# Optimization experiments

Hardware: AMD Instinct MI355X
Metric: run time of the kernel (lower is better)

Reference implementation:

```python
import jax, jax.numpy as jnp
import numpy as np

N, E, D, A, M, H, NRES = 65536, 16384, 1024, 512, 2048, 3, 3


def setup_inputs() -> dict:
    key = jax.random.key(0)
    ks = jax.random.split(key, 24)
    s = 0.02
    inp = {
        'h': jax.random.normal(ks[0], (N, D), dtype=jnp.float32),
        'rep': jax.random.normal(ks[1], (N, D), dtype=jnp.float32),
        'src': jax.random.randint(ks[2], (E,), 0, N, dtype=jnp.int32),
        'dst': jax.random.randint(ks[3], (E,), 0, N, dtype=jnp.int32),
        # per-head attention projections (stacked over H heads)
        'Wq': s * jax.random.normal(ks[4], (H, D, A), dtype=jnp.float32),
        'bq': s * jax.random.normal(ks[5], (H, A), dtype=jnp.float32),
        'Wk': s * jax.random.normal(ks[6], (H, D, A), dtype=jnp.float32),
        'bk': s * jax.random.normal(ks[7], (H, A), dtype=jnp.float32),
        'Wv': s * jax.random.normal(ks[8], (H, D, A), dtype=jnp.float32),
        'bv': s * jax.random.normal(ks[9], (H, A), dtype=jnp.float32),
        # MultiMLPLayer: first Linear(A->M), then NRES ResNet blocks of width M
        'W0': s * jax.random.normal(ks[10], (H, A, M), dtype=jnp.float32),
        'b0': s * jax.random.normal(ks[11], (H, M), dtype=jnp.float32),
        'Wr': s * jax.random.normal(ks[12], (H, NRES, M, M), dtype=jnp.float32),
        'br': s * jax.random.normal(ks[13], (H, NRES, M), dtype=jnp.float32),
        'g_ln': jnp.ones((H, NRES, M), dtype=jnp.float32),
        'b_ln': jnp.zeros((H, NRES, M), dtype=jnp.float32),
        # mlp_scale: Linear(M->A) per head
        'Wms': s * jax.random.normal(ks[14], (H, M, A), dtype=jnp.float32),
        'bms': s * jax.random.normal(ks[15], (H, A), dtype=jnp.float32),
        # update_attn_scale: Linear(H*A -> D, bias=False)
        'Wuas': s * jax.random.normal(ks[16], (H * A, D), dtype=jnp.float32),
    }
    return inp


def _layernorm(x, g, b, eps=1e-5):
    mu = jnp.mean(x, axis=-1, keepdims=True)
    var = jnp.mean((x - mu) ** 2, axis=-1, keepdims=True)
    return (x - mu) / jnp.sqrt(var + eps) * g + b


def reference(h, rep, src, dst, Wq, bq, Wk, bk, Wv, bv, W0, b0, Wr, br,
              g_ln, b_ln, Wms, bms, Wuas):
    # model normalizes all node embeddings first (F.normalize)
    hn = h / jnp.maximum(jnp.linalg.norm(h, axis=-1, keepdims=True), 1e-12)
    Q = hn[src]            # [E, D] mailbox messages (copy_u of 'h')
    K = rep[dst]           # [E, D] destination node reps (K == V)

    # per-head projections: [H, E, A]
    Qp = jnp.einsum('ed,hda->hea', Q, Wq) + bq[:, None, :]
    Kp = jnp.einsum('ed,hda->hea', K, Wk) + bk[:, None, :]
    Vp = jnp.einsum('ed,hda->hea', K, Wv) + bv[:, None, :]

    attn_dim = Wq.shape[-1]
    scores = (Qp * Kp) / (attn_dim ** 0.5)       # 2D path: elementwise QK, scaled by sqrt(attn_size)
    attn = jax.nn.softmax(scores, axis=-1)       # softmax over feature dim
    attn_out = attn * Vp                         # [H, E, A] (dropout p=0.0 in TreeHopNode)

    # MultiMLPLayer: Linear(A->M) then NRES ResNet blocks
    m = jnp.einsum('hea,ham->hem', attn_out, W0) + b0[:, None, :]
    for j in range(Wr.shape[1]):
        xn = _layernorm(m, g_ln[:, j][:, None, :], b_ln[:, j][:, None, :])
        m = m + jax.nn.relu(jnp.einsum('hem,hmn->hen', xn, Wr[:, j]) + br[:, j][:, None, :])

    head_out = jnp.einsum('hem,hma->hea', m, Wms) + bms[:, None, :] + attn_out  # [H, E, A]
    cat = jnp.transpose(head_out, (1, 0, 2)).reshape(Q.shape[0], -1)            # [E, H*A]

    # reduce_func: h = Q - K + update_attn_scale(multi_head_out)
    return Q - K + cat @ Wuas                                                   # [E, D]
```

## Files before the change

### kernel.cpp

```cpp
#include <hip/hip_runtime.h>
#include <hip/hip_bf16.h>
#include <cstdint>
#include <cstddef>

typedef __bf16 bf16;
typedef __bf16 bf16x2 __attribute__((ext_vector_type(2)));
typedef __bf16 bf16x4 __attribute__((ext_vector_type(4)));
typedef __bf16 bf16x8 __attribute__((ext_vector_type(8)));
typedef float f32x4 __attribute__((ext_vector_type(4)));

static_assert(sizeof(bf16x8) == 16, "bf16x8 must be 16B");

#define NE 16384
#define ND 1024
#define NA 512
#define NM 2048
#define NH 3
#define NRES 3
#define ESH 14

__device__ __forceinline__ void async_ld16(const bf16* g, bf16* l) {
  __builtin_amdgcn_global_load_lds(
      (__attribute__((address_space(1))) void*)(void*)g,
      (__attribute__((address_space(3))) void*)(void*)l, 16, 0, 0);
}

template <int N>
__device__ __forceinline__ void vm_wait() {
  asm volatile("s_waitcnt vmcnt(%0)" ::"n"(N) : "memory");
}
__device__ __forceinline__ void lgkm0() {
  asm volatile("s_waitcnt lgkmcnt(0)" ::: "memory");
}
__device__ __forceinline__ void bar() {
  asm volatile("s_barrier" ::: "memory");
}
#define PIN() __builtin_amdgcn_sched_barrier(0)


#define LDA_H(KS, BUF, MQ)                                                    \
  {                                                                           \
    const int ab_ = ((BUF)*2 + (MQ)) * 8192 + aOff;                           \
    const int co_ = (c0 ^ ((KS) << 2)) * 8;                                   \
    _Pragma("unroll") for (int i = 0; i < 4; ++i)                             \
        fa[KS][i] = *(const bf16x8*)&lA[ab_ + i * 1024 + co_];                \
  }

#define LDB_H(DST, KS, BUF, NQ)                                               \
  {                                                                           \
    const int bb_ = ((BUF)*2 + (NQ)) * 8192 + bOff;                           \
    const int co_ = (c0 ^ ((KS) << 2)) * 8;                                   \
    _Pragma("unroll") for (int j = 0; j < 2; ++j)                             \
        DST[KS][j] = *(const bf16x8*)&lB[bb_ + j * 1024 + co_];               \
  }

#define MFMA_H(KS, MQ, NQ, FB)                                                \
  __builtin_amdgcn_s_setprio(1);                                              \
  _Pragma("unroll") for (int i = 0; i < 4; ++i)                               \
  _Pragma("unroll") for (int j = 0; j < 2; ++j)                               \
      acc[(MQ)*4 + i][(NQ)*2 + j] = __builtin_amdgcn_mfma_f32_16x16x32_bf16(  \
          fa[KS][i], FB[KS][j], acc[(MQ)*4 + i][(NQ)*2 + j], 0, 0, 0);        \
  __builtin_amdgcn_s_setprio(0);

template <int MODE>
__global__ __launch_bounds__(512, 2) void gemm_kernel(
    const bf16* __restrict__ A, const bf16* __restrict__ B,
    const float* __restrict__ bias, void* __restrict__ Cv,
    const bf16* __restrict__ addb, int K, int ldc, int coloff, int addld,
    int nbx, int hsh, long long bstr, int bistr) {
  __shared__ bf16 lA[32768];
  __shared__ bf16 lB[32768];

  const int nwg = gridDim.x;
  int bid = blockIdx.x;
  if ((nwg & 7) == 0) bid = (bid & 7) * (nwg >> 3) + (bid >> 3);
  const int n0 = (bid % nbx) * 256;
  const int m0 = (bid / nbx) * 256;

  const int hidx = hsh ? (m0 >> hsh) : 0;
  if (hsh) {
    B += (size_t)hidx * (size_t)bstr;
    bias += (size_t)hidx * (size_t)bistr;
  }

  const int tid = threadIdx.x;
  const int wv = tid >> 6, ln = tid & 63;
  const int wm = wv >> 2, wn = wv & 3;

  const int rowq = wv * 8 + (ln >> 3);
  const int colo = ((ln & 7) ^ (ln >> 3)) * 8;
  const bf16* gA = A + (size_t)(m0 + rowq) * K + colo;
  const bf16* gB = B + (size_t)(n0 + rowq) * K + colo;

  auto stageA = [&](int bf, int u, int t) {
#pragma unroll
    for (int r = 0; r < 2; ++r)
      async_ld16(gA + (size_t)(r * 128 + u * 64) * K + t * 64,
                 &lA[((bf * 2 + u) * 128 + r * 64 + wv * 8) * 64]);
  };
  auto stageB = [&](int bf, int u, int t) {
#pragma unroll
    for (int r = 0; r < 2; ++r)
      async_ld16(gB + (size_t)(r * 128 + u * 64) * K + t * 64,
                 &lB[((bf * 2 + u) * 128 + r * 64 + wv * 8) * 64]);
  };

  const int l15 = ln & 15;
  const int aOff = (wm * 64 + l15) * 64;
  const int bOff = (wn * 32 + l15) * 64;
  const int c0 = (ln >> 4) ^ (ln & 7);

  f32x4 acc[8][4] = {};
  bf16x8 fa[2][4], fb0[2][2], fb1[2][2];

  const int nt = K >> 6;

  stageA(0, 0, 0); stageA(0, 1, 0); stageB(0, 0, 0); stageB(0, 1, 0);
  stageA(1, 0, 1); stageA(1, 1, 1); stageB(1, 0, 1); stageB(1, 1, 1);
  vm_wait<8>();
  bar();
  LDA_H(0, 0, 0); LDA_H(1, 0, 0); LDB_H(fb0, 0, 0, 0); LDB_H(fb0, 1, 0, 0);
  lgkm0();
  bar();

  for (int t = 0; t < nt; ++t) {
    const int buf = t & 1, nb = buf ^ 1;
    const bool s1 = t + 1 < nt, s2 = t + 2 < nt;
    if (s2) { stageB(buf, 0, t + 2); stageA(buf, 0, t + 2); }
    PIN();
    LDB_H(fb1, 0, buf, 1); LDB_H(fb1, 1, buf, 1);
    PIN();
    MFMA_H(0, 0, 0, fb0);
    MFMA_H(1, 0, 0, fb0);
    MFMA_H(0, 0, 1, fb1);
    PIN();
    LDA_H(0, buf, 1);
    PIN();
    MFMA_H(1, 0, 1, fb1);
    PIN();
    LDA_H(1, buf, 1);
    lgkm0();
    bar();
    if (s2) { stageB(buf, 1, t + 2); stageA(buf, 1, t + 2); }
    PIN();
    MFMA_H(0, 1, 1, fb1);
    MFMA_H(1, 1, 1, fb1);
    if (s2) { vm_wait<8>(); } else if (s1) { vm_wait<0>(); }
    bar();
    MFMA_H(0, 1, 0, fb0);
    PIN();
    if (s1) { LDB_H(fb0, 0, nb, 0); LDA_H(0, nb, 0); }
    PIN();
    MFMA_H(1, 1, 0, fb0);
    PIN();
    if (s1) { LDB_H(fb0, 1, nb, 0); LDA_H(1, nb, 0); }
    lgkm0();
    bar();
  }

  const int r4 = (ln >> 4) * 4;
  const int nbase = n0 + (wn >> 1) * 128 + (wn & 1) * 32 + l15;
#pragma unroll
  for (int mi = 0; mi < 8; ++mi) {
#pragma unroll
    for (int ni = 0; ni < 4; ++ni) {
#pragma unroll
      for (int r = 0; r < 4; ++r) {
        const int m = m0 + wm * 128 + mi * 16 + r4 + r;
        const int n = nbase + (ni >> 1) * 64 + (ni & 1) * 16;
        float v = acc[mi][ni][r];
        if constexpr (MODE != 3) v += bias[n];
        if constexpr (MODE == 0) {
          size_t idx = (size_t)m * ldc + n;
          if (coloff && n >= coloff) idx += (size_t)addld;
          ((bf16*)Cv)[idx] = (bf16)v;
        } else if constexpr (MODE == 1) {
          float prev = (float)addb[(size_t)m * addld + n];
          ((bf16*)Cv)[(size_t)m * ldc + n] = (bf16)(prev + fmaxf(v, 0.f));
        } else if constexpr (MODE == 2) {
          v += (float)addb[(size_t)m * addld + n];
          const int mloc = hsh ? (m & ((1 << hsh) - 1)) : m;
          ((bf16*)Cv)[(size_t)mloc * ldc + hidx * coloff + n] = (bf16)v;
        } else {
          float* C = (float*)Cv;
          const size_t idx = (size_t)m * ldc + n;
          C[idx] = C[idx] + v;
        }
      }
    }
  }
}

template <int MODE>
static void launch_gemm(hipStream_t s, const bf16* A, const bf16* B,
                        const float* bias, void* C, const bf16* addb, int M,
                        int N, int K, int ldc, int coloff, int addld,
                        int hsh = 0, long long bstr = 0, int bistr = 0) {
  const int nbx = N / 256;
  gemm_kernel<MODE><<<dim3(nbx * (M / 256)), 512, 0, s>>>(
      A, B, bias, C, addb, K, ldc, coloff, addld, nbx, hsh, bstr, bistr);
}

__global__ void transpose_cvt(const float* __restrict__ src,
                              bf16* __restrict__ dst, int K, int N) {
  __shared__ float t[32][33];
  const size_t zo = (size_t)blockIdx.z * K * N;
  src += zo;
  dst += zo;
  const int n = blockIdx.x * 32 + threadIdx.x;
  const int kb = blockIdx.y * 32;
#pragma unroll
  for (int i = 0; i < 4; ++i) {
    const int k = kb + threadIdx.y + i * 8;
    t[threadIdx.y + i * 8][threadIdx.x] = src[(size_t)k * N + n];
  }
  __syncthreads();
#pragma unroll
  for (int i = 0; i < 4; ++i) {
    const int nn = blockIdx.x * 32 + threadIdx.y + i * 8;
    dst[(size_t)nn * K + kb + threadIdx.x] =
        (bf16)t[threadIdx.x][threadIdx.y + i * 8];
  }
}

__global__ void concat2_kernel(const float* __restrict__ a,
                               const float* __restrict__ b,
                               float* __restrict__ dst, int na) {
  const int i = blockIdx.x * 256 + threadIdx.x;
  dst[i] = (i < na) ? a[i] : b[i - na];
}

__global__ __launch_bounds__(256) void gather_kernel(
    const float* __restrict__ h, const float* __restrict__ rep,
    const int* __restrict__ src, const int* __restrict__ dst,
    bf16* __restrict__ Qb, bf16* __restrict__ Kb, float* __restrict__ qk) {
  __shared__ float sm[4];
  const int e = blockIdx.x, tid = threadIdx.x;
  const int sr = src[e], dr = dst[e];
  const float4 hv = ((const float4*)(h + (size_t)sr * ND))[tid];
  float ss = hv.x * hv.x + hv.y * hv.y + hv.z * hv.z + hv.w * hv.w;
#pragma unroll
  for (int o = 32; o > 0; o >>= 1) ss += __shfl_down(ss, o, 64);
  if ((tid & 63) == 0) sm[tid >> 6] = ss;
  __syncthreads();
  const float tot = sm[0] + sm[1] + sm[2] + sm[3];
  const float inv = 1.f / fmaxf(sqrtf(tot), 1e-12f);
  const float4 rv = ((const float4*)(rep + (size_t)dr * ND))[tid];
  const float q0 = hv.x * inv, q1 = hv.y * inv, q2 = hv.z * inv,
              q3 = hv.w * inv;
  const size_t base = (size_t)e * ND + tid * 4;
  bf16x4 qv;
  qv[0] = (bf16)q0; qv[1] = (bf16)q1; qv[2] = (bf16)q2; qv[3] = (bf16)q3;
  *(bf16x4*)(Qb + base) = qv;
  bf16x4 kv;
  kv[0] = (bf16)rv.x; kv[1] = (bf16)rv.y; kv[2] = (bf16)rv.z;
  kv[3] = (bf16)rv.w;
  *(bf16x4*)(Kb + base) = kv;
  *(float4*)(qk + base) =
      make_float4(q0 - rv.x, q1 - rv.y, q2 - rv.z, q3 - rv.w);
}

__global__ __launch_bounds__(256) void softmax_kernel(
    const bf16* __restrict__ Qp, const bf16* __restrict__ Kp,
    const bf16* __restrict__ Vp, bf16* __restrict__ attn) {
  __shared__ float sm[4];
  const int tid = threadIdx.x;
  const int e = blockIdx.x, hh = blockIdx.y;
  const size_t base = (size_t)e * (NH * NA) + (size_t)hh * NA + 2 * tid;
  const bf16x2 q = *(const bf16x2*)(Qp + base);
  const bf16x2 k = *(const bf16x2*)(Kp + base);
  const bf16x2 v = *(const bf16x2*)(Vp + base);
  const float sc = 0.044194173824159216f;
  const float s0 = (float)q[0] * (float)k[0] * sc;
  const float s1 = (float)q[1] * (float)k[1] * sc;
  float mx = fmaxf(s0, s1);
#pragma unroll
  for (int o = 32; o > 0; o >>= 1) mx = fmaxf(mx, __shfl_down(mx, o, 64));
  if ((tid & 63) == 0) sm[tid >> 6] = mx;
  __syncthreads();
  mx = fmaxf(fmaxf(sm[0], sm[1]), fmaxf(sm[2], sm[3]));
  __syncthreads();
  const float p0 = expf(s0 - mx), p1 = expf(s1 - mx);
  float ssum = p0 + p1;
#pragma unroll
  for (int o = 32; o > 0; o >>= 1) ssum += __shfl_down(ssum, o, 64);
  if ((tid & 63) == 0) sm[tid >> 6] = ssum;
  __syncthreads();
  const float inv = 1.f / (sm[0] + sm[1] + sm[2] + sm[3]);
  bf16x2 r;
  r[0] = (bf16)(p0 * inv * (float)v[0]);
  r[1] = (bf16)(p1 * inv * (float)v[1]);
  const size_t obase = (size_t)hh * NE * NA + (size_t)e * NA + 2 * tid;
  *(bf16x2*)(attn + obase) = r;
}

__global__ __launch_bounds__(256) void ln_kernel(const bf16* __restrict__ x,
                                                 bf16* __restrict__ y,
                                                 const float* __restrict__ g,
                                                 const float* __restrict__ b) {
  __shared__ float sm[8];
  const int tid = threadIdx.x;
  const size_t base = (size_t)blockIdx.x * NM + tid * 8;
  const bf16x8 xv = *(const bf16x8*)(x + base);
  float xf[8], s = 0.f, ss = 0.f;
#pragma unroll
  for (int i = 0; i < 8; ++i) {
    xf[i] = (float)xv[i];
    s += xf[i];
    ss += xf[i] * xf[i];
  }
#pragma unroll
  for (int o = 32; o > 0; o >>= 1) {
    s += __shfl_down(s, o, 64);
    ss += __shfl_down(ss, o, 64);
  }
  if ((tid & 63) == 0) {
    sm[tid >> 6] = s;
    sm[4 + (tid >> 6)] = ss;
  }
  __syncthreads();
  s = sm[0] + sm[1] + sm[2] + sm[3];
  ss = sm[4] + sm[5] + sm[6] + sm[7];
  const float mu = s * (1.f / NM);
  const float var = ss * (1.f / NM) - mu * mu;
  const float rstd = rsqrtf(fmaxf(var, 0.f) + 1e-5f);
  const int c0 = tid * 8;
  bf16x8 yv;
#pragma unroll
  for (int i = 0; i < 8; ++i)
    yv[i] = (bf16)((xf[i] - mu) * rstd * g[c0 + i] + b[c0 + i]);
  *(bf16x8*)(y + base) = yv;
}

extern "C" void kernel_launch(void* const* d_in, const int* in_sizes, int n_in,
                              void* d_out, int out_size, void* d_ws,
                              size_t ws_size, hipStream_t stream) {
  const float* h    = (const float*)d_in[0];
  const float* rep  = (const float*)d_in[1];
  const int* src    = (const int*)d_in[2];
  const int* dst    = (const int*)d_in[3];
  const float* Wq   = (const float*)d_in[4];
  const float* bq   = (const float*)d_in[5];
  const float* Wk   = (const float*)d_in[6];
  const float* bk   = (const float*)d_in[7];
  const float* Wv   = (const float*)d_in[8];
  const float* bv   = (const float*)d_in[9];
  const float* W0   = (const float*)d_in[10];
  const float* b0   = (const float*)d_in[11];
  const float* Wr   = (const float*)d_in[12];
  const float* br   = (const float*)d_in[13];
  const float* g_ln = (const float*)d_in[14];
  const float* b_ln = (const float*)d_in[15];
  const float* Wms  = (const float*)d_in[16];
  const float* bms  = (const float*)d_in[17];
  const float* Wuas = (const float*)d_in[18];
  float* out = (float*)d_out;

  bf16* ws = (bf16*)d_ws;
  size_t off = 0;
  auto alloc = [&](size_t n) {
    bf16* p = ws + off;
    off += n;
    return p;
  };
  bf16* WqT   = alloc((size_t)NH * NA * ND);
  bf16* WkT   = alloc((size_t)NH * NA * ND);
  bf16* WvT   = alloc((size_t)NH * NA * ND);
  bf16* W0T   = alloc((size_t)NH * NM * NA);
  bf16* WrT   = alloc((size_t)NH * NRES * NM * NM);
  bf16* WmsT  = alloc((size_t)NH * NA * NM);
  bf16* WuasT = alloc((size_t)ND * NH * NA);
  bf16* Qb    = alloc((size_t)NE * ND);
  bf16* Kb    = alloc((size_t)NE * ND);
  bf16* Qp    = alloc((size_t)NE * NH * NA);
  bf16* Kp    = alloc((size_t)NE * NH * NA);
  bf16* Vp    = alloc((size_t)NE * NH * NA);
  bf16* attn  = alloc((size_t)NH * NE * NA);
  bf16* mbuf3 = alloc((size_t)NH * NE * NM);
  bf16* xnb   = alloc((size_t)NE * NM);
  float* cbias = (float*)alloc(2 * (size_t)NH * NA * 2);
  bf16* cat   = Qp;
  if (ws_size < off * sizeof(bf16)) return;

  const dim3 tb(32, 8);
  transpose_cvt<<<dim3(NA / 32, ND / 32, NH), tb, 0, stream>>>(Wq, WqT, ND, NA);
  transpose_cvt<<<dim3(NA / 32, ND / 32, NH), tb, 0, stream>>>(Wk, WkT, ND, NA);
  transpose_cvt<<<dim3(NA / 32, ND / 32, NH), tb, 0, stream>>>(Wv, WvT, ND, NA);
  transpose_cvt<<<dim3(NM / 32, NA / 32, NH), tb, 0, stream>>>(W0, W0T, NA, NM);
  transpose_cvt<<<dim3(NM / 32, NM / 32, NH * NRES), tb, 0, stream>>>(Wr, WrT,
                                                                      NM, NM);
  transpose_cvt<<<dim3(NA / 32, NM / 32, NH), tb, 0, stream>>>(Wms, WmsT, NM,
                                                               NA);
  transpose_cvt<<<dim3(ND / 32, (NH * NA) / 32, 1), tb, 0, stream>>>(
      Wuas, WuasT, NH * NA, ND);
  concat2_kernel<<<(2 * NH * NA) / 256, 256, 0, stream>>>(bk, bv, cbias,
                                                          NH * NA);

  gather_kernel<<<NE, 256, 0, stream>>>(h, rep, src, dst, Qb, Kb, out);

  launch_gemm<0>(stream, Qb, WqT, bq, Qp, nullptr, NE, NH * NA, ND, NH * NA,
                 0, 0);
  launch_gemm<0>(stream, Kb, WkT, cbias, Kp, nullptr, NE, 2 * NH * NA, ND,
                 NH * NA, NH * NA, (NE - 1) * NH * NA);
  softmax_kernel<<<dim3(NE, NH), 256, 0, stream>>>(Qp, Kp, Vp, attn);

  for (int hh = 0; hh < NH; ++hh) {
    const bf16* attn_h = attn + (size_t)hh * NE * NA;
    bf16* mbuf_h = mbuf3 + (size_t)hh * NE * NM;
    launch_gemm<0>(stream, attn_h, W0T + (size_t)hh * NM * NA, b0 + hh * NM,
                   mbuf_h, nullptr, NE, NM, NA, NM, 0, 0);
    for (int j = 0; j < NRES; ++j) {
      const int hj = hh * NRES + j;
      ln_kernel<<<NE, 256, 0, stream>>>(mbuf_h, xnb, g_ln + (size_t)hj * NM,
                                        b_ln + (size_t)hj * NM);
      launch_gemm<1>(stream, xnb, WrT + (size_t)hj * NM * NM, br + hj * NM,
                     mbuf_h, mbuf_h, NE, NM, NM, NM, 0, NM);
    }
  }
  launch_gemm<2>(stream, mbuf3, WmsT, bms, cat, attn, NH * NE, NA, NM,
                 NH * NA, NA, NA, ESH, (long long)NA * NM, NA);

  launch_gemm<3>(stream, cat, WuasT, nullptr, out, nullptr, NE, ND, NH * NA,
                 ND, 0, 0);
}
```

Measured before the change: 2.606 ms.

## Fold LayerNorm into ResNet GEMMs via weight scaling and epilogue row statistics

Removes the standalone LayerNorm kernel. Gamma is folded into the transposed Wr weights, and mean and beta are folded into precomputed column sums (sgW and bWbr). The GEMM epilogue applies rstd*(acc - mu*sgW) + bWbr, using per-row sum and sum-of-squares that the previous GEMM epilogue accumulates with atomics. This drops a full read and write of the activation buffer per residual block, at the cost of atomic traffic in the epilogue. It also adds numerical risk, since the raw un-normalized bf16 activations now feed the MFMA.

```diff
diff --git a/kernel.cpp b/kernel.cpp
--- a/kernel.cpp
+++ b/kernel.cpp
@@ -67,7 +67,9 @@
     const bf16* __restrict__ A, const bf16* __restrict__ B,
     const float* __restrict__ bias, void* __restrict__ Cv,
     const bf16* __restrict__ addb, int K, int ldc, int coloff, int addld,
-    int nbx, int hsh, long long bstr, int bistr) {
+    int nbx, int hsh, long long bstr, int bistr,
+    const float* __restrict__ lnbb, const float* __restrict__ stats_in,
+    float* __restrict__ stats_out) {
   __shared__ bf16 lA[32768];
   __shared__ bf16 lB[32768];
 
@@ -163,21 +165,34 @@
 #pragma unroll
   for (int mi = 0; mi < 8; ++mi) {
 #pragma unroll
-    for (int ni = 0; ni < 4; ++ni) {
-#pragma unroll
-      for (int r = 0; r < 4; ++r) {
-        const int m = m0 + wm * 128 + mi * 16 + r4 + r;
+    for (int r = 0; r < 4; ++r) {
+      const int m = m0 + wm * 128 + mi * 16 + r4 + r;
+      float mu = 0.f, rstd = 0.f;
+      if constexpr (MODE == 1) {
+        const float2 st = *(const float2*)&stats_in[2 * m];
+        mu = st.x * (1.f / NM);
+        const float var = st.y * (1.f / NM) - mu * mu;
+        rstd = rsqrtf(fmaxf(var, 0.f) + 1e-5f);
+      }
+      float s = 0.f, sq = 0.f;
+#pragma unroll
+      for (int ni = 0; ni < 4; ++ni) {
         const int n = nbase + (ni >> 1) * 64 + (ni & 1) * 16;
         float v = acc[mi][ni][r];
-        if constexpr (MODE != 3) v += bias[n];
         if constexpr (MODE == 0) {
+          v += bias[n];
           size_t idx = (size_t)m * ldc + n;
           if (coloff && n >= coloff) idx += (size_t)addld;
           ((bf16*)Cv)[idx] = (bf16)v;
+          s += v; sq += v * v;
         } else if constexpr (MODE == 1) {
-          float prev = (float)addb[(size_t)m * addld + n];
-          ((bf16*)Cv)[(size_t)m * ldc + n] = (bf16)(prev + fmaxf(v, 0.f));
+          v = rstd * (v - mu * bias[n]) + lnbb[n];
+          const float prev = (float)addb[(size_t)m * addld + n];
+          const float y = prev + fmaxf(v, 0.f);
+          ((bf16*)Cv)[(size_t)m * ldc + n] = (bf16)y;
+          s += y; sq += y * y;
         } else if constexpr (MODE == 2) {
+          v += bias[n];
           v += (float)addb[(size_t)m * addld + n];
           const int mloc = hsh ? (m & ((1 << hsh) - 1)) : m;
           ((bf16*)Cv)[(size_t)mloc * ldc + hidx * coloff + n] = (bf16)v;
@@ -187,6 +202,19 @@
           C[idx] = C[idx] + v;
         }
       }
+      if constexpr (MODE <= 1) {
+        if (stats_out) {
+#pragma unroll
+          for (int o = 1; o < 16; o <<= 1) {
+            s += __shfl_xor(s, o, 64);
+            sq += __shfl_xor(sq, o, 64);
+          }
+          if (l15 == 0) {
+            atomicAdd(&stats_out[2 * m], s);
+            atomicAdd(&stats_out[2 * m + 1], sq);
+          }
+        }
+      }
     }
   }
 }
@@ -195,16 +223,22 @@
 static void launch_gemm(hipStream_t s, const bf16* A, const bf16* B,
                         const float* bias, void* C, const bf16* addb, int M,
                         int N, int K, int ldc, int coloff, int addld,
-                        int hsh = 0, long long bstr = 0, int bistr = 0) {
+                        int hsh = 0, long long bstr = 0, int bistr = 0,
+                        const float* lnbb = nullptr,
+                        const float* stats_in = nullptr,
+                        float* stats_out = nullptr) {
   const int nbx = N / 256;
   gemm_kernel<MODE><<<dim3(nbx * (M / 256)), 512, 0, s>>>(
-      A, B, bias, C, addb, K, ldc, coloff, addld, nbx, hsh, bstr, bistr);
+      A, B, bias, C, addb, K, ldc, coloff, addld, nbx, hsh, bstr, bistr,
+      lnbb, stats_in, stats_out);
 }
 
 __global__ void transpose_cvt(const float* __restrict__ src,
-                              bf16* __restrict__ dst, int K, int N) {
+                              bf16* __restrict__ dst, int K, int N,
+                              const float* __restrict__ scale) {
   __shared__ float t[32][33];
-  const size_t zo = (size_t)blockIdx.z * K * N;
+  const int z = blockIdx.z;
+  const size_t zo = (size_t)z * K * N;
   src += zo;
   dst += zo;
   const int n = blockIdx.x * 32 + threadIdx.x;
@@ -215,12 +249,37 @@
     t[threadIdx.y + i * 8][threadIdx.x] = src[(size_t)k * N + n];
   }
   __syncthreads();
+  const float sc = scale ? scale[(size_t)z * K + kb + threadIdx.x] : 1.f;
 #pragma unroll
   for (int i = 0; i < 4; ++i) {
     const int nn = blockIdx.x * 32 + threadIdx.y + i * 8;
     dst[(size_t)nn * K + kb + threadIdx.x] =
-        (bf16)t[threadIdx.x][threadIdx.y + i * 8];
-  }
+        (bf16)(t[threadIdx.x][threadIdx.y + i * 8] * sc);
+  }
+}
+
+__global__ void lnfold_kernel(const float* __restrict__ Wr,
+                              const float* __restrict__ g,
+                              const float* __restrict__ b,
+                              const float* __restrict__ br,
+                              float* __restrict__ sgW,
+                              float* __restrict__ bWbr) {
+  const int hj = blockIdx.y;
+  const int n = blockIdx.x * 256 + threadIdx.x;
+  const float* W = Wr + (size_t)hj * NM * NM;
+  float sg = 0.f, sb = 0.f;
+  for (int k = 0; k < NM; ++k) {
+    const float w = W[(size_t)k * NM + n];
+    sg += g[hj * NM + k] * w;
+    sb += b[hj * NM + k] * w;
+  }
+  sgW[hj * NM + n] = sg;
+  bWbr[hj * NM + n] = sb + br[hj * NM + n];
+}
+
+__global__ void zerof_kernel(float* __restrict__ p, int n) {
+  const int i = blockIdx.x * 256 + threadIdx.x;
+  if (i < n) p[i] = 0.f;
 }
 
 __global__ void concat2_kernel(const float* __restrict__ a,
@@ -292,44 +351,6 @@
   r[1] = (bf16)(p1 * inv * (float)v[1]);
   const size_t obase = (size_t)hh * NE * NA + (size_t)e * NA + 2 * tid;
   *(bf16x2*)(attn + obase) = r;
-}
-
-__global__ __launch_bounds__(256) void ln_kernel(const bf16* __restrict__ x,
-                                                 bf16* __restrict__ y,
-                                                 const float* __restrict__ g,
-                                                 const float* __restrict__ b) {
-  __shared__ float sm[8];
-  const int tid = threadIdx.x;
-  const size_t base = (size_t)blockIdx.x * NM + tid * 8;
-  const bf16x8 xv = *(const bf16x8*)(x + base);
-  float xf[8], s = 0.f, ss = 0.f;
-#pragma unroll
-  for (int i = 0; i < 8; ++i) {
-    xf[i] = (float)xv[i];
-    s += xf[i];
-    ss += xf[i] * xf[i];
-  }
-#pragma unroll
-  for (int o = 32; o > 0; o >>= 1) {
-    s += __shfl_down(s, o, 64);
-    ss += __shfl_down(ss, o, 64);
-  }
-  if ((tid & 63) == 0) {
-    sm[tid >> 6] = s;
-    sm[4 + (tid >> 6)] = ss;
-  }
-  __syncthreads();
-  s = sm[0] + sm[1] + sm[2] + sm[3];
-  ss = sm[4] + sm[5] + sm[6] + sm[7];
-  const float mu = s * (1.f / NM);
-  const float var = ss * (1.f / NM) - mu * mu;
-  const float rstd = rsqrtf(fmaxf(var, 0.f) + 1e-5f);
-  const int c0 = tid * 8;
-  bf16x8 yv;
-#pragma unroll
-  for (int i = 0; i < 8; ++i)
-    yv[i] = (bf16)((xf[i] - mu) * rstd * g[c0 + i] + b[c0 + i]);
-  *(bf16x8*)(y + base) = yv;
 }
 
 extern "C" void kernel_launch(void* const* d_in, const int* in_sizes, int n_in,
@@ -377,24 +398,33 @@
   bf16* Vp    = alloc((size_t)NE * NH * NA);
   bf16* attn  = alloc((size_t)NH * NE * NA);
   bf16* mbuf3 = alloc((size_t)NH * NE * NM);
-  bf16* xnb   = alloc((size_t)NE * NM);
-  float* cbias = (float*)alloc(2 * (size_t)NH * NA * 2);
+  float* cbias  = (float*)alloc(2 * (size_t)NH * NA * 2);
+  float* sgW    = (float*)alloc((size_t)NH * NRES * NM * 2);
+  float* bWbr   = (float*)alloc((size_t)NH * NRES * NM * 2);
+  float* stats9 = (float*)alloc((size_t)9 * NE * 2 * 2);
   bf16* cat   = Qp;
   if (ws_size < off * sizeof(bf16)) return;
 
   const dim3 tb(32, 8);
-  transpose_cvt<<<dim3(NA / 32, ND / 32, NH), tb, 0, stream>>>(Wq, WqT, ND, NA);
-  transpose_cvt<<<dim3(NA / 32, ND / 32, NH), tb, 0, stream>>>(Wk, WkT, ND, NA);
-  transpose_cvt<<<dim3(NA / 32, ND / 32, NH), tb, 0, stream>>>(Wv, WvT, ND, NA);
-  transpose_cvt<<<dim3(NM / 32, NA / 32, NH), tb, 0, stream>>>(W0, W0T, NA, NM);
-  transpose_cvt<<<dim3(NM / 32, NM / 32, NH * NRES), tb, 0, stream>>>(Wr, WrT,
-                                                                      NM, NM);
+  transpose_cvt<<<dim3(NA / 32, ND / 32, NH), tb, 0, stream>>>(Wq, WqT, ND, NA,
+                                                               nullptr);
+  transpose_cvt<<<dim3(NA / 32, ND / 32, NH), tb, 0, stream>>>(Wk, WkT, ND, NA,
+                                                               nullptr);
+  transpose_cvt<<<dim3(NA / 32, ND / 32, NH), tb, 0, stream>>>(Wv, WvT, ND, NA,
+                                                               nullptr);
+  transpose_cvt<<<dim3(NM / 32, NA / 32, NH), tb, 0, stream>>>(W0, W0T, NA, NM,
+                                                               nullptr);
+  transpose_cvt<<<dim3(NM / 32, NM / 32, NH * NRES), tb, 0, stream>>>(
+      Wr, WrT, NM, NM, g_ln);
   transpose_cvt<<<dim3(NA / 32, NM / 32, NH), tb, 0, stream>>>(Wms, WmsT, NM,
-                                                               NA);
+                                                               NA, nullptr);
   transpose_cvt<<<dim3(ND / 32, (NH * NA) / 32, 1), tb, 0, stream>>>(
-      Wuas, WuasT, NH * NA, ND);
+      Wuas, WuasT, NH * NA, ND, nullptr);
   concat2_kernel<<<(2 * NH * NA) / 256, 256, 0, stream>>>(bk, bv, cbias,
                                                           NH * NA);
+  lnfold_kernel<<<dim3(NM / 256, NH * NRES), 256, 0, stream>>>(
+      Wr, g_ln, b_ln, br, sgW, bWbr);
+  zerof_kernel<<<(9 * NE * 2) / 256, 256, 0, stream>>>(stats9, 9 * NE * 2);
 
   gather_kernel<<<NE, 256, 0, stream>>>(h, rep, src, dst, Qb, Kb, out);
 
@@ -407,14 +437,18 @@
   for (int hh = 0; hh < NH; ++hh) {
     const bf16* attn_h = attn + (size_t)hh * NE * NA;
     bf16* mbuf_h = mbuf3 + (size_t)hh * NE * NM;
+    float* S[3] = {stats9 + (size_t)(hh * 3 + 0) * NE * 2,
+                   stats9 + (size_t)(hh * 3 + 1) * NE * 2,
+                   stats9 + (size_t)(hh * 3 + 2) * NE * 2};
     launch_gemm<0>(stream, attn_h, W0T + (size_t)hh * NM * NA, b0 + hh * NM,
-                   mbuf_h, nullptr, NE, NM, NA, NM, 0, 0);
+                   mbuf_h, nullptr, NE, NM, NA, NM, 0, 0, 0, 0, 0, nullptr,
+                   nullptr, S[0]);
     for (int j = 0; j < NRES; ++j) {
       const int hj = hh * NRES + j;
-      ln_kernel<<<NE, 256, 0, stream>>>(mbuf_h, xnb, g_ln + (size_t)hj * NM,
-                                        b_ln + (size_t)hj * NM);
-      launch_gemm<1>(stream, xnb, WrT + (size_t)hj * NM * NM, br + hj * NM,
-                     mbuf_h, mbuf_h, NE, NM, NM, NM, 0, NM);
+      launch_gemm<1>(stream, mbuf_h, WrT + (size_t)hj * NM * NM,
+                     sgW + (size_t)hj * NM, mbuf_h, mbuf_h, NE, NM, NM, NM, 0,
+                     NM, 0, 0, 0, bWbr + (size_t)hj * NM, S[j],
+                     j + 1 < NRES ? S[j + 1] : nullptr);
     }
   }
   launch_gemm<2>(stream, mbuf3, WmsT, bms, cat, attn, NH * NE, NA, NM,
```

New measurement: 2.960 ms. 13.6% more time.

## Replace 256x256 pipelined GEMM with simpler 128x128 single-buffered tile kernel

Applied to the files above, without the earlier changes.

Replaces the hand-scheduled 256x256 tile, 8-wave, double-buffered GEMM with a 128x128 tile, 4-wave kernel. It uses a single LDS buffer, with a full vmcnt wait and barrier each K step. The intent appears to be more workgroups per CU and simpler scheduling in exchange for less data reuse per tile. The risk is that global loads and MFMA no longer overlap well, and the fine-grained interleaving that hid LDS latency is gone.

```diff
diff --git a/kernel.cpp b/kernel.cpp
--- a/kernel.cpp
+++ b/kernel.cpp
@@ -35,47 +35,22 @@
 __device__ __forceinline__ void bar() {
   asm volatile("s_barrier" ::: "memory");
 }
-#define PIN() __builtin_amdgcn_sched_barrier(0)
-
-
-#define LDA_H(KS, BUF, MQ)                                                    \
-  {                                                                           \
-    const int ab_ = ((BUF)*2 + (MQ)) * 8192 + aOff;                           \
-    const int co_ = (c0 ^ ((KS) << 2)) * 8;                                   \
-    _Pragma("unroll") for (int i = 0; i < 4; ++i)                             \
-        fa[KS][i] = *(const bf16x8*)&lA[ab_ + i * 1024 + co_];                \
-  }
-
-#define LDB_H(DST, KS, BUF, NQ)                                               \
-  {                                                                           \
-    const int bb_ = ((BUF)*2 + (NQ)) * 8192 + bOff;                           \
-    const int co_ = (c0 ^ ((KS) << 2)) * 8;                                   \
-    _Pragma("unroll") for (int j = 0; j < 2; ++j)                             \
-        DST[KS][j] = *(const bf16x8*)&lB[bb_ + j * 1024 + co_];               \
-  }
-
-#define MFMA_H(KS, MQ, NQ, FB)                                                \
-  __builtin_amdgcn_s_setprio(1);                                              \
-  _Pragma("unroll") for (int i = 0; i < 4; ++i)                               \
-  _Pragma("unroll") for (int j = 0; j < 2; ++j)                               \
-      acc[(MQ)*4 + i][(NQ)*2 + j] = __builtin_amdgcn_mfma_f32_16x16x32_bf16(  \
-          fa[KS][i], FB[KS][j], acc[(MQ)*4 + i][(NQ)*2 + j], 0, 0, 0);        \
-  __builtin_amdgcn_s_setprio(0);
+
 
 template <int MODE>
-__global__ __launch_bounds__(512, 2) void gemm_kernel(
+__global__ __launch_bounds__(256, 3) void gemm_kernel(
     const bf16* __restrict__ A, const bf16* __restrict__ B,
     const float* __restrict__ bias, void* __restrict__ Cv,
     const bf16* __restrict__ addb, int K, int ldc, int coloff, int addld,
     int nbx, int hsh, long long bstr, int bistr) {
-  __shared__ bf16 lA[32768];
-  __shared__ bf16 lB[32768];
+  __shared__ bf16 lA[8192];
+  __shared__ bf16 lB[8192];
 
   const int nwg = gridDim.x;
   int bid = blockIdx.x;
   if ((nwg & 7) == 0) bid = (bid & 7) * (nwg >> 3) + (bid >> 3);
-  const int n0 = (bid % nbx) * 256;
-  const int m0 = (bid / nbx) * 256;
+  const int n0 = (bid % nbx) * 128;
+  const int m0 = (bid / nbx) * 128;
 
   const int hidx = hsh ? (m0 >> hsh) : 0;
   if (hsh) {
@@ -85,89 +60,73 @@
 
   const int tid = threadIdx.x;
   const int wv = tid >> 6, ln = tid & 63;
-  const int wm = wv >> 2, wn = wv & 3;
+  const int wm = wv >> 1, wn = wv & 1;
 
   const int rowq = wv * 8 + (ln >> 3);
   const int colo = ((ln & 7) ^ (ln >> 3)) * 8;
   const bf16* gA = A + (size_t)(m0 + rowq) * K + colo;
   const bf16* gB = B + (size_t)(n0 + rowq) * K + colo;
 
-  auto stageA = [&](int bf, int u, int t) {
-#pragma unroll
-    for (int r = 0; r < 2; ++r)
-      async_ld16(gA + (size_t)(r * 128 + u * 64) * K + t * 64,
-                 &lA[((bf * 2 + u) * 128 + r * 64 + wv * 8) * 64]);
-  };
-  auto stageB = [&](int bf, int u, int t) {
-#pragma unroll
-    for (int r = 0; r < 2; ++r)
-      async_ld16(gB + (size_t)(r * 128 + u * 64) * K + t * 64,
-                 &lB[((bf * 2 + u) * 128 + r * 64 + wv * 8) * 64]);
+  auto stage = [&](int t) {
+#pragma unroll
+    for (int r = 0; r < 4; ++r) {
+      async_ld16(gA + (size_t)(r * 32) * K + t * 64,
+                 &lA[(r * 32 + wv * 8) * 64]);
+      async_ld16(gB + (size_t)(r * 32) * K + t * 64,
+                 &lB[(r * 32 + wv * 8) * 64]);
+    }
   };
 
   const int l15 = ln & 15;
   const int aOff = (wm * 64 + l15) * 64;
-  const int bOff = (wn * 32 + l15) * 64;
+  const int bOff = (wn * 64 + l15) * 64;
   const int c0 = (ln >> 4) ^ (ln & 7);
 
-  f32x4 acc[8][4] = {};
-  bf16x8 fa[2][4], fb0[2][2], fb1[2][2];
+  f32x4 acc[4][4] = {};
+  bf16x8 fa[2][4], fb[2][4];
 
   const int nt = K >> 6;
 
-  stageA(0, 0, 0); stageA(0, 1, 0); stageB(0, 0, 0); stageB(0, 1, 0);
-  stageA(1, 0, 1); stageA(1, 1, 1); stageB(1, 0, 1); stageB(1, 1, 1);
-  vm_wait<8>();
-  bar();
-  LDA_H(0, 0, 0); LDA_H(1, 0, 0); LDB_H(fb0, 0, 0, 0); LDB_H(fb0, 1, 0, 0);
-  lgkm0();
-  bar();
+  stage(0);
 
   for (int t = 0; t < nt; ++t) {
-    const int buf = t & 1, nb = buf ^ 1;
-    const bool s1 = t + 1 < nt, s2 = t + 2 < nt;
-    if (s2) { stageB(buf, 0, t + 2); stageA(buf, 0, t + 2); }
-    PIN();
-    LDB_H(fb1, 0, buf, 1); LDB_H(fb1, 1, buf, 1);
-    PIN();
-    MFMA_H(0, 0, 0, fb0);
-    MFMA_H(1, 0, 0, fb0);
-    MFMA_H(0, 0, 1, fb1);
-    PIN();
-    LDA_H(0, buf, 1);
-    PIN();
-    MFMA_H(1, 0, 1, fb1);
-    PIN();
-    LDA_H(1, buf, 1);
+    vm_wait<0>();
+    bar();
+#pragma unroll
+    for (int ks = 0; ks < 2; ++ks) {
+      const int co = (c0 ^ (ks << 2)) * 8;
+#pragma unroll
+      for (int i = 0; i < 4; ++i)
+        fa[ks][i] = *(const bf16x8*)&lA[aOff + i * 1024 + co];
+#pragma unroll
+      for (int j = 0; j < 4; ++j)
+        fb[ks][j] = *(const bf16x8*)&lB[bOff + j * 1024 + co];
+    }
     lgkm0();
     bar();
-    if (s2) { stageB(buf, 1, t + 2); stageA(buf, 1, t + 2); }
-    PIN();
-    MFMA_H(0, 1, 1, fb1);
-    MFMA_H(1, 1, 1, fb1);
-    if (s2) { vm_wait<8>(); } else if (s1) { vm_wait<0>(); }
-    bar();
-    MFMA_H(0, 1, 0, fb0);
-    PIN();
-    if (s1) { LDB_H(fb0, 0, nb, 0); LDA_H(0, nb, 0); }
-    PIN();
-    MFMA_H(1, 1, 0, fb0);
-    PIN();
-    if (s1) { LDB_H(fb0, 1, nb, 0); LDA_H(1, nb, 0); }
-    lgkm0();
-    bar();
+    if (t + 1 < nt) stage(t + 1);
+    __builtin_amdgcn_s_setprio(1);
+#pragma unroll
+    for (int ks = 0; ks < 2; ++ks)
+#pragma unroll
+      for (int i = 0; i < 4; ++i)
+#pragma unroll
+        for (int j = 0; j < 4; ++j)
+          acc[i][j] = __builtin_amdgcn_mfma_f32_16x16x32_bf16(
+              fa[ks][i], fb[ks][j], acc[i][j], 0, 0, 0);
+    __builtin_amdgcn_s_setprio(0);
   }
 
   const int r4 = (ln >> 4) * 4;
-  const int nbase = n0 + (wn >> 1) * 128 + (wn & 1) * 32 + l15;
-#pragma unroll
-  for (int mi = 0; mi < 8; ++mi) {
-#pragma unroll
-    for (int ni = 0; ni < 4; ++ni) {
-#pragma unroll
-      for (int r = 0; r < 4; ++r) {
-        const int m = m0 + wm * 128 + mi * 16 + r4 + r;
-        const int n = nbase + (ni >> 1) * 64 + (ni & 1) * 16;
+  const int nbase = n0 + wn * 64 + l15;
+#pragma unroll
+  for (int mi = 0; mi < 4; ++mi) {
+#pragma unroll
+    for (int r = 0; r < 4; ++r) {
+      const int m = m0 + wm * 64 + mi * 16 + r4 + r;
+#pragma unroll
+      for (int ni = 0; ni < 4; ++ni) {
+        const int n = nbase + ni * 16;
         float v = acc[mi][ni][r];
         if constexpr (MODE != 3) v += bias[n];
         if constexpr (MODE == 0) {
@@ -196,8 +155,8 @@
                         const float* bias, void* C, const bf16* addb, int M,
                         int N, int K, int ldc, int coloff, int addld,
                         int hsh = 0, long long bstr = 0, int bistr = 0) {
-  const int nbx = N / 256;
-  gemm_kernel<MODE><<<dim3(nbx * (M / 256)), 512, 0, s>>>(
+  const int nbx = N / 128;
+  gemm_kernel<MODE><<<dim3(nbx * (M / 128)), 256, 0, s>>>(
       A, B, bias, C, addb, K, ldc, coloff, addld, nbx, hsh, bstr, bistr);
 }
 
```

Result: faster. 2.550 ms (-2.2%).
